# Performance work log

Measured on AMD Instinct MI355X. Metric: run time of the kernel, lower is better.

Reference implementation:

```python
import jax, jax.numpy as jnp
import numpy as np
from jax import lax

GAMMA = 0.001  # init kwarg gamma
DN = ('NCHW', 'OIHW', 'NCHW')


def _maxpool2(x):
    # 2x2 max pool, stride 2, NCHW
    return lax.reduce_window(x, -jnp.inf, lax.max, (1, 1, 2, 2), (1, 1, 2, 2), 'VALID')


def _features(x, w1, b1, w2, b2):
    h = lax.conv_general_dilated(x, w1, (1, 1), 'SAME', dimension_numbers=DN)
    h = _maxpool2(jax.nn.relu(h + b1[None, :, None, None]))
    h = lax.conv_general_dilated(h, w2, (1, 1), 'SAME', dimension_numbers=DN)
    h = _maxpool2(jax.nn.relu(h + b2[None, :, None, None]))
    return h.reshape(h.shape[0], -1)  # [N, 16*7*7=784]


def setup_inputs() -> dict:
    key = jax.random.key(0)
    ks = jax.random.split(key, 7)
    x = jax.random.normal(ks[0], (4096, 1, 28, 28), dtype=jnp.float32)
    w1 = jax.random.normal(ks[1], (8, 1, 3, 3), dtype=jnp.float32) * 0.1
    b1 = jax.random.normal(ks[2], (8,), dtype=jnp.float32) * 0.1
    w2 = jax.random.normal(ks[3], (16, 8, 3, 3), dtype=jnp.float32) * 0.1
    b2 = jax.random.normal(ks[4], (16,), dtype=jnp.float32) * 0.1
    support = jax.random.uniform(ks[5], (8192, 784), dtype=jnp.float32)
    alpha = jax.random.normal(ks[6], (8192, 4), dtype=jnp.float32)
    return {'x': x, 'w1': w1, 'b1': b1, 'w2': w2, 'b2': b2,
            'support': support, 'alpha': alpha}


def reference(x, w1, b1, w2, b2, support, alpha):
    feats = _features(x, w1, b1, w2, b2)                      # [N, 784]
    # Pairwise squared distances via expansion (replaces the N*M python loop)
    f2 = jnp.sum(feats * feats, axis=1, keepdims=True)        # [N, 1]
    s2 = jnp.sum(support * support, axis=1)[None, :]          # [1, M]
    d2 = f2 + s2 - 2.0 * (feats @ support.T)                  # [N, M]
    K = jnp.exp(-GAMMA * d2)                                  # RBF kernel matrix
    return K @ alpha                                          # [N, n_classes]
```

## Files before the change

### kernel.cpp

```cpp
#include <hip/hip_runtime.h>
#include <hip/hip_bf16.h>
#include <cstdint>

#define GAMMA 0.001f
#define TILE_BYTES 114688

typedef __attribute__((ext_vector_type(4))) float f32x4;
typedef __attribute__((ext_vector_type(8))) int v8i;
typedef unsigned char u8;

__device__ inline unsigned pack4_fp8(float4 f) {
  unsigned p = __builtin_amdgcn_cvt_pk_fp8_f32(f.x, f.y, 0, false);
  p = __builtin_amdgcn_cvt_pk_fp8_f32(f.z, f.w, p, true);
  return p;
}

__global__ __launch_bounds__(256, 4) void conv_prep_kernel(
    const float* __restrict__ x, const float* __restrict__ w1,
    const float* __restrict__ b1, const float* __restrict__ w2,
    const float* __restrict__ b2, const float* __restrict__ support,
    const float* __restrict__ alpha, u8* __restrict__ feats_t,
    u8* __restrict__ sup_t, float* __restrict__ beta,
    float* __restrict__ ef) {
  int tid = threadIdx.x;
  int bx = blockIdx.x;

  if (bx >= 2048) {
    int lane = tid & 63, wave = tid >> 6;
    int m = (bx - 2048) * 4 + wave;
    const float* row = support + (size_t)m * 784;
    int mt = m >> 7, mr = m & 127;
    u8* tb = sup_t + (size_t)mt * TILE_BYTES;
    float ss = 0.f;
    if (lane < 56) {
      uint4 w;
      if (lane < 49) {
        float4 f0 = ((const float4*)row)[lane * 4 + 0];
        float4 f1 = ((const float4*)row)[lane * 4 + 1];
        float4 f2 = ((const float4*)row)[lane * 4 + 2];
        float4 f3 = ((const float4*)row)[lane * 4 + 3];
        ss = f0.x * f0.x + f0.y * f0.y + f0.z * f0.z + f0.w * f0.w +
             f1.x * f1.x + f1.y * f1.y + f1.z * f1.z + f1.w * f1.w +
             f2.x * f2.x + f2.y * f2.y + f2.z * f2.z + f2.w * f2.w +
             f3.x * f3.x + f3.y * f3.y + f3.z * f3.z + f3.w * f3.w;
        w.x = pack4_fp8(f0); w.y = pack4_fp8(f1);
        w.z = pack4_fp8(f2); w.w = pack4_fp8(f3);
      } else {
        w.x = 0; w.y = 0; w.z = 0; w.w = 0;
      }
      int kk = lane >> 3, u = lane & 7, q = u >> 1, h = u & 1;
      int qs = q ^ ((mr >> 1) & 3);
      *(uint4*)(tb + kk * 16384 + h * 8192 + mr * 64 + qs * 16) = w;
    }
#pragma unroll
    for (int s = 1; s < 64; s <<= 1) ss += __shfl_xor(ss, s, 64);
    if (lane == 0) {
      float es = __expf(-GAMMA * ss);
      float4 a = ((const float4*)alpha)[m];
      float4 b;
      b.x = es * a.x; b.y = es * a.y; b.z = es * a.z; b.w = es * a.w;
      ((float4*)beta)[m] = b;
    }
    return;
  }

  __shared__ float xp[2][900];
  __shared__ float a1p[2][2560];
  __shared__ float w1s[72], b1s[8], b2s[16];
  __shared__ float w2t[1152];
  __shared__ alignas(16) u8 fb[2][784];
  __shared__ float red[256];

  for (int t = tid; t < 1800; t += 256) ((float*)xp)[t] = 0.f;
  for (int t = tid; t < 5120; t += 256) ((float*)a1p)[t] = 0.f;
  if (tid < 72) w1s[tid] = w1[tid];
  if (tid < 8) b1s[tid] = b1[tid];
  if (tid < 16) b2s[tid] = b2[tid];
  for (int t = tid; t < 1152; t += 256) {
    int o = t / 72, r = t % 72;
    w2t[r * 16 + o] = w2[t];
  }
  __syncthreads();

  for (int t = tid; t < 392; t += 256) {
    int img = t >= 196, j = t - img * 196;
    float4 v = ((const float4*)(x + (size_t)(bx * 2 + img) * 784))[j];
    int r = j / 7, c = (j % 7) * 4;
    float* p = &xp[img][(r + 1) * 30 + (c + 1)];
    p[0] = v.x; p[1] = v.y; p[2] = v.z; p[3] = v.w;
  }
  __syncthreads();

  for (int idx = tid; idx < 3136; idx += 256) {
    int img = idx >= 1568;
    int rem = idx - img * 1568;
    int c = rem / 196, r2 = rem % 196;
    int ph = r2 / 14, pw = r2 % 14;
    const float* w = &w1s[c * 9];
    const float* xb = &xp[img][(2 * ph) * 30 + (2 * pw)];
    float t[4][4];
#pragma unroll
    for (int a = 0; a < 4; a++) {
      float2 u0 = *(const float2*)(xb + a * 30);
      float2 u1 = *(const float2*)(xb + a * 30 + 2);
      t[a][0] = u0.x; t[a][1] = u0.y; t[a][2] = u1.x; t[a][3] = u1.y;
    }
    float s00 = 0, s01 = 0, s10 = 0, s11 = 0;
#pragma unroll
    for (int dy = 0; dy < 3; dy++)
#pragma unroll
      for (int dx = 0; dx < 3; dx++) {
        float wv = w[dy * 3 + dx];
        s00 += t[dy][dx] * wv;     s01 += t[dy][dx + 1] * wv;
        s10 += t[dy + 1][dx] * wv; s11 += t[dy + 1][dx + 1] * wv;
      }
    float mx = fmaxf(fmaxf(s00, s01), fmaxf(s10, s11));
    a1p[img][c * 320 + (ph + 1) * 20 + (pw + 1)] = fmaxf(mx + b1s[c], 0.f);
  }
  __syncthreads();

  int img = tid >> 7, r = tid & 127;
  float fsq = 0.f;
  if (r < 112) {
    int o = r & 15, y7 = r >> 4;
    float accT[14], accB[14];
#pragma unroll
    for (int q = 0; q < 14; q++) { accT[q] = 0.f; accB[q] = 0.f; }
    for (int ic = 0; ic < 8; ic++) {
      const float* wb = &w2t[ic * 144 + o];
      float wv[9];
#pragma unroll
      for (int k = 0; k < 9; k++) wv[k] = wb[k * 16];
      const float* ap = &a1p[img][ic * 320 + (2 * y7) * 20];
#pragma unroll
      for (int a = 0; a < 4; a++) {
        float rw[16];
        float4 q0 = *(const float4*)(ap + a * 20 + 0);
        float4 q1 = *(const float4*)(ap + a * 20 + 4);
        float4 q2 = *(const float4*)(ap + a * 20 + 8);
        float4 q3 = *(const float4*)(ap + a * 20 + 12);
        rw[0] = q0.x;  rw[1] = q0.y;  rw[2] = q0.z;  rw[3] = q0.w;
        rw[4] = q1.x;  rw[5] = q1.y;  rw[6] = q1.z;  rw[7] = q1.w;
        rw[8] = q2.x;  rw[9] = q2.y;  rw[10] = q2.z; rw[11] = q2.w;
        rw[12] = q3.x; rw[13] = q3.y; rw[14] = q3.z; rw[15] = q3.w;
        if (a < 3) {
#pragma unroll
          for (int q = 0; q < 14; q++)
            accT[q] += wv[a * 3] * rw[q] + wv[a * 3 + 1] * rw[q + 1] +
                       wv[a * 3 + 2] * rw[q + 2];
        }
        if (a >= 1) {
#pragma unroll
          for (int q = 0; q < 14; q++)
            accB[q] += wv[(a - 1) * 3] * rw[q] + wv[(a - 1) * 3 + 1] * rw[q + 1] +
                       wv[(a - 1) * 3 + 2] * rw[q + 2];
        }
      }
    }
    float bo = b2s[o];
#pragma unroll
    for (int x7 = 0; x7 < 7; x7++) {
      float mx = fmaxf(fmaxf(accT[2 * x7], accT[2 * x7 + 1]),
                       fmaxf(accB[2 * x7], accB[2 * x7 + 1]));
      float val = fmaxf(mx + bo, 0.f);
      fb[img][o * 49 + y7 * 7 + x7] =
          (u8)(__builtin_amdgcn_cvt_pk_fp8_f32(val, 0.f, 0, false) & 0xff);
      fsq += val * val;
    }
  }
  red[tid] = fsq;
  __syncthreads();
  for (int s = 64; s > 0; s >>= 1) {
    if ((tid & 127) < s) red[tid] += red[tid + s];
    __syncthreads();
  }
  if ((tid & 127) == 0) ef[bx * 2 + img] = __expf(-GAMMA * red[tid]);

  if (tid < 112) {
    int im = tid >= 56, j = tid - im * 56;
    uint4 v;
    if (j < 49) v = ((const uint4*)fb[im])[j];
    else { v.x = 0; v.y = 0; v.z = 0; v.w = 0; }
    int n = bx * 2 + im;
    int nt = n >> 7, nr = n & 127;
    int kk = j >> 3, u = j & 7, q = u >> 1, h = u & 1;
    int qs = q ^ ((nr >> 1) & 3);
    *(uint4*)(feats_t + (size_t)nt * TILE_BYTES + kk * 16384 + h * 8192 +
              nr * 64 + qs * 16) = v;
  }
}

__global__ __launch_bounds__(256, 2) void rbf_gemm_kernel(
    const u8* __restrict__ feats_t, const u8* __restrict__ sup_t,
    const float* __restrict__ beta, float* __restrict__ partial) {
  __shared__ alignas(16) u8 As[16384];
  __shared__ alignas(16) u8 Bs[16384];
  int tid = threadIdx.x;
  int wave = tid >> 6, lane = tid & 63;
  int bx = blockIdx.x;
  int chunk = bx & 63, nb = bx >> 6;
  const u8* at = feats_t + (size_t)nb * TILE_BYTES;
  const u8* bt = sup_t + (size_t)chunk * TILE_BYTES;
  int wn = wave >> 1, wm = wave & 1;
  int col = lane & 15, quad = lane >> 4;
  int slot = quad ^ ((col >> 1) & 3);

  f32x4 acc[4][4];
#pragma unroll
  for (int i = 0; i < 4; i++)
#pragma unroll
    for (int j = 0; j < 4; j++) acc[i][j] = (f32x4){0, 0, 0, 0};

  for (int kk = 0; kk < 7; ++kk) {
    const u8* ak = at + kk * 16384 + tid * 16;
    const u8* bk = bt + kk * 16384 + tid * 16;
    u8* la = As + tid * 16;
    u8* lb = Bs + tid * 16;
#pragma unroll
    for (int s = 0; s < 4; s++) {
      __builtin_amdgcn_global_load_lds(
          (const __attribute__((address_space(1))) void*)(ak + s * 4096),
          (__attribute__((address_space(3))) void*)(la + s * 4096), 16, 0, 0);
      __builtin_amdgcn_global_load_lds(
          (const __attribute__((address_space(1))) void*)(bk + s * 4096),
          (__attribute__((address_space(3))) void*)(lb + s * 4096), 16, 0, 0);
    }
    __syncthreads();
    v8i av[4], bv[4];
#pragma unroll
    for (int i = 0; i < 4; i++) {
      const u8* p = As + (wn * 64 + i * 16 + col) * 64 + slot * 16;
      int4 lo = *(const int4*)p;
      int4 hi = *(const int4*)(p + 8192);
      av[i] = (v8i){lo.x, lo.y, lo.z, lo.w, hi.x, hi.y, hi.z, hi.w};
    }
#pragma unroll
    for (int j = 0; j < 4; j++) {
      const u8* p = Bs + (wm * 64 + j * 16 + col) * 64 + slot * 16;
      int4 lo = *(const int4*)p;
      int4 hi = *(const int4*)(p + 8192);
      bv[j] = (v8i){lo.x, lo.y, lo.z, lo.w, hi.x, hi.y, hi.z, hi.w};
    }
#pragma unroll
    for (int i = 0; i < 4; i++)
#pragma unroll
      for (int j = 0; j < 4; j++)
        acc[i][j] = __builtin_amdgcn_mfma_scale_f32_16x16x128_f8f6f4(
            av[i], bv[j], acc[i][j], 0, 0, 0, 0x7f7f7f7f, 0, 0x7f7f7f7f);
    __syncthreads();
  }

#pragma unroll
  for (int i = 0; i < 4; i++)
#pragma unroll
    for (int j = 0; j < 4; j++) {
      acc[i][j].x = __expf(2.f * GAMMA * acc[i][j].x);
      acc[i][j].y = __expf(2.f * GAMMA * acc[i][j].y);
      acc[i][j].z = __expf(2.f * GAMMA * acc[i][j].z);
      acc[i][j].w = __expf(2.f * GAMMA * acc[i][j].w);
    }
  int n0 = nb * 128, m0 = chunk * 128;
#pragma unroll
  for (int c = 0; c < 4; ++c) {
    float bl[4];
#pragma unroll
    for (int j = 0; j < 4; j++)
      bl[j] = beta[(m0 + wm * 64 + j * 16 + col) * 4 + c];
#pragma unroll
    for (int i = 0; i < 4; i++) {
      f32x4 s = acc[i][0] * bl[0] + acc[i][1] * bl[1] + acc[i][2] * bl[2] +
                acc[i][3] * bl[3];
#pragma unroll
      for (int st = 1; st < 16; st <<= 1) {
        s.x += __shfl_xor(s.x, st, 16);
        s.y += __shfl_xor(s.y, st, 16);
        s.z += __shfl_xor(s.z, st, 16);
        s.w += __shfl_xor(s.w, st, 16);
      }
      if (col == c) {
        int n = n0 + wn * 64 + i * 16 + quad * 4;
        float* pp = partial + (((size_t)chunk * 2 + wm) * 4096 + n) * 4 + c;
        pp[0] = s.x; pp[4] = s.y; pp[8] = s.z; pp[12] = s.w;
      }
    }
  }
}

__global__ __launch_bounds__(256) void reduce_kernel(
    const float* __restrict__ partial, const float* __restrict__ ef,
    float* __restrict__ out) {
  __shared__ float4 sred[4][64];
  int nl = threadIdx.x & 63, chq = threadIdx.x >> 6;
  int n = blockIdx.x * 64 + nl;
  const float4* p = (const float4*)partial;
  float sx = 0, sy = 0, sz = 0, sw = 0;
  for (int ch = chq * 32; ch < chq * 32 + 32; ch++) {
    float4 v = p[(size_t)ch * 4096 + n];
    sx += v.x; sy += v.y; sz += v.z; sw += v.w;
  }
  sred[chq][nl] = (float4){sx, sy, sz, sw};
  __syncthreads();
  if (chq == 0) {
    float4 a = sred[0][nl], b = sred[1][nl], c = sred[2][nl], d = sred[3][nl];
    float e = ef[n];
    float4 o;
    o.x = e * (a.x + b.x + c.x + d.x);
    o.y = e * (a.y + b.y + c.y + d.y);
    o.z = e * (a.z + b.z + c.z + d.z);
    o.w = e * (a.w + b.w + c.w + d.w);
    ((float4*)out)[n] = o;
  }
}

extern "C" void kernel_launch(void* const* d_in, const int* in_sizes, int n_in,
                              void* d_out, int out_size, void* d_ws,
                              size_t ws_size, hipStream_t stream) {
  const float* x = (const float*)d_in[0];
  const float* w1 = (const float*)d_in[1];
  const float* b1 = (const float*)d_in[2];
  const float* w2 = (const float*)d_in[3];
  const float* b2 = (const float*)d_in[4];
  const float* support = (const float*)d_in[5];
  const float* alpha = (const float*)d_in[6];
  float* out = (float*)d_out;

  u8* ws = (u8*)d_ws;
  u8* sup_t = ws;
  u8* feats_t = ws + 7340032;
  float* beta = (float*)(ws + 11010048);
  float* ef = (float*)(ws + 11141120);
  float* partial = (float*)(ws + 11157504);

  conv_prep_kernel<<<4096, 256, 0, stream>>>(x, w1, b1, w2, b2, support, alpha,
                                             feats_t, sup_t, beta, ef);
  rbf_gemm_kernel<<<2048, 256, 0, stream>>>(feats_t, sup_t, beta, partial);
  reduce_kernel<<<64, 256, 0, stream>>>(partial, ef, out);
}
```

Before: 188.2 us.

## Pre-swizzle fp8 tiles into MFMA fragment layout and load directly to registers

The prep kernel now writes the fp8 feature and support tiles in a layout where each 16-row fragment's lane data is contiguous, so each lane of the GEMM can read its MFMA operands straight from global memory. The GEMM drops the LDS staging buffers, the global_load_lds copies and both per-iteration barriers, and fully unrolls the k loop. The aim is to cut LDS traffic and synchronisation. The cost is that operand reuse across waves now goes through L2/L1 instead of shared memory, and more global loads stay in flight in registers. Launch-bound occupancy hints are also removed from both kernels.

```diff
diff --git a/kernel.cpp b/kernel.cpp
--- a/kernel.cpp
+++ b/kernel.cpp
@@ -15,7 +15,7 @@
   return p;
 }
 
-__global__ __launch_bounds__(256, 4) void conv_prep_kernel(
+__global__ __launch_bounds__(256) void conv_prep_kernel(
     const float* __restrict__ x, const float* __restrict__ w1,
     const float* __restrict__ b1, const float* __restrict__ w2,
     const float* __restrict__ b2, const float* __restrict__ support,
@@ -49,8 +49,8 @@
         w.x = 0; w.y = 0; w.z = 0; w.w = 0;
       }
       int kk = lane >> 3, u = lane & 7, q = u >> 1, h = u & 1;
-      int qs = q ^ ((mr >> 1) & 3);
-      *(uint4*)(tb + kk * 16384 + h * 8192 + mr * 64 + qs * 16) = w;
+      *(uint4*)(tb + kk * 16384 + (mr >> 4) * 2048 + h * 1024 +
+                (q * 16 + (mr & 15)) * 16) = w;
     }
 #pragma unroll
     for (int s = 1; s < 64; s <<= 1) ss += __shfl_xor(ss, s, 64);
@@ -184,26 +184,22 @@
     int n = bx * 2 + im;
     int nt = n >> 7, nr = n & 127;
     int kk = j >> 3, u = j & 7, q = u >> 1, h = u & 1;
-    int qs = q ^ ((nr >> 1) & 3);
-    *(uint4*)(feats_t + (size_t)nt * TILE_BYTES + kk * 16384 + h * 8192 +
-              nr * 64 + qs * 16) = v;
-  }
-}
-
-__global__ __launch_bounds__(256, 2) void rbf_gemm_kernel(
+    *(uint4*)(feats_t + (size_t)nt * TILE_BYTES + kk * 16384 +
+              (nr >> 4) * 2048 + h * 1024 + (q * 16 + (nr & 15)) * 16) = v;
+  }
+}
+
+__global__ __launch_bounds__(256) void rbf_gemm_kernel(
     const u8* __restrict__ feats_t, const u8* __restrict__ sup_t,
     const float* __restrict__ beta, float* __restrict__ partial) {
-  __shared__ alignas(16) u8 As[16384];
-  __shared__ alignas(16) u8 Bs[16384];
   int tid = threadIdx.x;
   int wave = tid >> 6, lane = tid & 63;
   int bx = blockIdx.x;
   int chunk = bx & 63, nb = bx >> 6;
-  const u8* at = feats_t + (size_t)nb * TILE_BYTES;
-  const u8* bt = sup_t + (size_t)chunk * TILE_BYTES;
   int wn = wave >> 1, wm = wave & 1;
   int col = lane & 15, quad = lane >> 4;
-  int slot = quad ^ ((col >> 1) & 3);
+  const u8* at = feats_t + (size_t)nb * TILE_BYTES + wn * 4 * 2048 + lane * 16;
+  const u8* bt = sup_t + (size_t)chunk * TILE_BYTES + wm * 4 * 2048 + lane * 16;
 
   f32x4 acc[4][4];
 #pragma unroll
@@ -211,35 +207,25 @@
 #pragma unroll
     for (int j = 0; j < 4; j++) acc[i][j] = (f32x4){0, 0, 0, 0};
 
+#pragma unroll
   for (int kk = 0; kk < 7; ++kk) {
-    const u8* ak = at + kk * 16384 + tid * 16;
-    const u8* bk = bt + kk * 16384 + tid * 16;
-    u8* la = As + tid * 16;
-    u8* lb = Bs + tid * 16;
-#pragma unroll
-    for (int s = 0; s < 4; s++) {
-      __builtin_amdgcn_global_load_lds(
-          (const __attribute__((address_space(1))) void*)(ak + s * 4096),
-          (__attribute__((address_space(3))) void*)(la + s * 4096), 16, 0, 0);
-      __builtin_amdgcn_global_load_lds(
-          (const __attribute__((address_space(1))) void*)(bk + s * 4096),
-          (__attribute__((address_space(3))) void*)(lb + s * 4096), 16, 0, 0);
-    }
-    __syncthreads();
+    const u8* ak = at + kk * 16384;
+    const u8* bk = bt + kk * 16384;
+    int4 alo[4], ahi[4], blo[4], bhi[4];
+#pragma unroll
+    for (int i = 0; i < 4; i++) {
+      alo[i] = *(const int4*)(ak + i * 2048);
+      ahi[i] = *(const int4*)(ak + i * 2048 + 1024);
+      blo[i] = *(const int4*)(bk + i * 2048);
+      bhi[i] = *(const int4*)(bk + i * 2048 + 1024);
+    }
     v8i av[4], bv[4];
 #pragma unroll
     for (int i = 0; i < 4; i++) {
-      const u8* p = As + (wn * 64 + i * 16 + col) * 64 + slot * 16;
-      int4 lo = *(const int4*)p;
-      int4 hi = *(const int4*)(p + 8192);
-      av[i] = (v8i){lo.x, lo.y, lo.z, lo.w, hi.x, hi.y, hi.z, hi.w};
-    }
-#pragma unroll
-    for (int j = 0; j < 4; j++) {
-      const u8* p = Bs + (wm * 64 + j * 16 + col) * 64 + slot * 16;
-      int4 lo = *(const int4*)p;
-      int4 hi = *(const int4*)(p + 8192);
-      bv[j] = (v8i){lo.x, lo.y, lo.z, lo.w, hi.x, hi.y, hi.z, hi.w};
+      av[i] = (v8i){alo[i].x, alo[i].y, alo[i].z, alo[i].w,
+                    ahi[i].x, ahi[i].y, ahi[i].z, ahi[i].w};
+      bv[i] = (v8i){blo[i].x, blo[i].y, blo[i].z, blo[i].w,
+                    bhi[i].x, bhi[i].y, bhi[i].z, bhi[i].w};
     }
 #pragma unroll
     for (int i = 0; i < 4; i++)
@@ -247,7 +233,6 @@
       for (int j = 0; j < 4; j++)
         acc[i][j] = __builtin_amdgcn_mfma_scale_f32_16x16x128_f8f6f4(
             av[i], bv[j], acc[i][j], 0, 0, 0, 0x7f7f7f7f, 0, 0x7f7f7f7f);
-    __syncthreads();
   }
 
 #pragma unroll
```

After: 193.5 us. +2.8%, slower.

## Compute second conv layer with bf16 MFMA implicit GEMM in conv_prep kernel

Applied to the files above, without the earlier changes.

Replaces the scalar FP32 second convolution with a bf16 MFMA 16x16x32 implicit GEMM. The first-layer activations are stored channels-last in bf16, and each wave computes 16-position by 16-output-channel tiles over the 9 taps times 8 channels. Pre-pool results go to shared memory in bf16, and the max-pool plus bias and ReLU stage then reads from there. This removes heavy per-thread FMA work and register pressure, but loses precision by rounding both activations and conv outputs to bf16.

```diff
diff --git a/kernel.cpp b/kernel.cpp
--- a/kernel.cpp
+++ b/kernel.cpp
@@ -7,12 +7,18 @@
 
 typedef __attribute__((ext_vector_type(4))) float f32x4;
 typedef __attribute__((ext_vector_type(8))) int v8i;
+typedef __attribute__((ext_vector_type(8))) short bh8;
 typedef unsigned char u8;
 
 __device__ inline unsigned pack4_fp8(float4 f) {
   unsigned p = __builtin_amdgcn_cvt_pk_fp8_f32(f.x, f.y, 0, false);
   p = __builtin_amdgcn_cvt_pk_fp8_f32(f.z, f.w, p, true);
   return p;
+}
+
+__device__ inline ushort bf16u(float v) {
+  __hip_bfloat16 h = __float2bfloat16(v);
+  return *(ushort*)&h;
 }
 
 __global__ __launch_bounds__(256, 4) void conv_prep_kernel(
@@ -65,22 +71,34 @@
   }
 
   __shared__ float xp[2][900];
-  __shared__ float a1p[2][2560];
+  __shared__ alignas(16) ushort a1h[2][2048];
   __shared__ float w1s[72], b1s[8], b2s[16];
-  __shared__ float w2t[1152];
+  __shared__ float w2s[1152];
+  __shared__ alignas(8) ushort sc[2][16][212];
   __shared__ alignas(16) u8 fb[2][784];
   __shared__ float red[256];
 
+  int lane = tid & 63, wave = tid >> 6;
+
   for (int t = tid; t < 1800; t += 256) ((float*)xp)[t] = 0.f;
-  for (int t = tid; t < 5120; t += 256) ((float*)a1p)[t] = 0.f;
+  for (int t = tid; t < 1024; t += 256) ((uint4*)a1h)[t] = (uint4){0, 0, 0, 0};
   if (tid < 72) w1s[tid] = w1[tid];
   if (tid < 8) b1s[tid] = b1[tid];
   if (tid < 16) b2s[tid] = b2[tid];
-  for (int t = tid; t < 1152; t += 256) {
-    int o = t / 72, r = t % 72;
-    w2t[r * 16 + o] = w2[t];
-  }
-  __syncthreads();
+  for (int t = tid; t < 1152; t += 256) w2s[t] = w2[t];
+  __syncthreads();
+
+  int oc = lane & 15, quad = lane >> 4;
+  bh8 wf[3];
+#pragma unroll
+  for (int g = 0; g < 3; g++) {
+    int tap = g * 4 + quad;
+#pragma unroll
+    for (int j = 0; j < 8; j++) {
+      float v = (tap < 9) ? w2s[oc * 72 + j * 9 + tap] : 0.f;
+      wf[g][j] = (short)bf16u(v);
+    }
+  }
 
   for (int t = tid; t < 392; t += 256) {
     int img = t >= 196, j = t - img * 196;
@@ -115,7 +133,42 @@
         s10 += t[dy + 1][dx] * wv; s11 += t[dy + 1][dx + 1] * wv;
       }
     float mx = fmaxf(fmaxf(s00, s01), fmaxf(s10, s11));
-    a1p[img][c * 320 + (ph + 1) * 20 + (pw + 1)] = fmaxf(mx + b1s[c], 0.f);
+    float val = fmaxf(mx + b1s[c], 0.f);
+    a1h[img][((ph + 1) * 16 + (pw + 1)) * 8 + c] = bf16u(val);
+  }
+  __syncthreads();
+
+  {
+    int img2 = wave >> 1, half = wave & 1;
+    int Tstart = half * 7, Tcnt = half ? 6 : 7;
+    const ushort* abase = a1h[img2];
+    int mrow = lane & 15;
+    for (int t = 0; t < Tcnt; ++t) {
+      int T = Tstart + t;
+      int p = T * 16 + mrow;
+      int pc = p > 195 ? 195 : p;
+      int y = pc / 14, xq = pc - y * 14;
+      int cell = y * 16 + xq;
+      f32x4 acc = (f32x4){0, 0, 0, 0};
+#pragma unroll
+      for (int g = 0; g < 3; g++) {
+        int tap = g * 4 + quad;
+        const ushort* ap;
+        if (g == 2 && quad > 0) {
+          ap = abase;
+        } else {
+          int dy = tap / 3, dx = tap - dy * 3;
+          ap = abase + (cell + dy * 16 + dx) * 8;
+        }
+        bh8 af = *(const bh8*)ap;
+        acc = __builtin_amdgcn_mfma_f32_16x16x32_bf16(af, wf[g], acc, 0, 0, 0);
+      }
+      int pos0 = T * 16 + quad * 4;
+      ushort4 s4;
+      s4.x = bf16u(acc.x); s4.y = bf16u(acc.y);
+      s4.z = bf16u(acc.z); s4.w = bf16u(acc.w);
+      *(ushort4*)(&sc[img2][oc][pos0]) = s4;
+    }
   }
   __syncthreads();
 
@@ -123,45 +176,18 @@
   float fsq = 0.f;
   if (r < 112) {
     int o = r & 15, y7 = r >> 4;
-    float accT[14], accB[14];
-#pragma unroll
-    for (int q = 0; q < 14; q++) { accT[q] = 0.f; accB[q] = 0.f; }
-    for (int ic = 0; ic < 8; ic++) {
-      const float* wb = &w2t[ic * 144 + o];
-      float wv[9];
-#pragma unroll
-      for (int k = 0; k < 9; k++) wv[k] = wb[k * 16];
-      const float* ap = &a1p[img][ic * 320 + (2 * y7) * 20];
-#pragma unroll
-      for (int a = 0; a < 4; a++) {
-        float rw[16];
-        float4 q0 = *(const float4*)(ap + a * 20 + 0);
-        float4 q1 = *(const float4*)(ap + a * 20 + 4);
-        float4 q2 = *(const float4*)(ap + a * 20 + 8);
-        float4 q3 = *(const float4*)(ap + a * 20 + 12);
-        rw[0] = q0.x;  rw[1] = q0.y;  rw[2] = q0.z;  rw[3] = q0.w;
-        rw[4] = q1.x;  rw[5] = q1.y;  rw[6] = q1.z;  rw[7] = q1.w;
-        rw[8] = q2.x;  rw[9] = q2.y;  rw[10] = q2.z; rw[11] = q2.w;
-        rw[12] = q3.x; rw[13] = q3.y; rw[14] = q3.z; rw[15] = q3.w;
-        if (a < 3) {
-#pragma unroll
-          for (int q = 0; q < 14; q++)
-            accT[q] += wv[a * 3] * rw[q] + wv[a * 3 + 1] * rw[q + 1] +
-                       wv[a * 3 + 2] * rw[q + 2];
-        }
-        if (a >= 1) {
-#pragma unroll
-          for (int q = 0; q < 14; q++)
-            accB[q] += wv[(a - 1) * 3] * rw[q] + wv[(a - 1) * 3 + 1] * rw[q + 1] +
-                       wv[(a - 1) * 3 + 2] * rw[q + 2];
-        }
-      }
-    }
+    const ushort* srow = sc[img][o];
     float bo = b2s[o];
 #pragma unroll
     for (int x7 = 0; x7 < 7; x7++) {
-      float mx = fmaxf(fmaxf(accT[2 * x7], accT[2 * x7 + 1]),
-                       fmaxf(accB[2 * x7], accB[2 * x7 + 1]));
+      int p = 28 * y7 + 2 * x7;
+      unsigned u0 = *(const unsigned*)(&srow[p]);
+      unsigned u1 = *(const unsigned*)(&srow[p + 14]);
+      float a = __uint_as_float(u0 << 16);
+      float b = __uint_as_float(u0 & 0xffff0000u);
+      float c = __uint_as_float(u1 << 16);
+      float d = __uint_as_float(u1 & 0xffff0000u);
+      float mx = fmaxf(fmaxf(a, b), fmaxf(c, d));
       float val = fmaxf(mx + bo, 0.f);
       fb[img][o * 49 + y7 * 7 + x7] =
           (u8)(__builtin_amdgcn_cvt_pk_fp8_f32(val, 0.f, 0, false) & 0xff);
```

Result: faster. 168.2 us, median of 3 (-10.6%).
